# Kernel tuning notes

Hardware: AMD Instinct MI355X
Metric: run time of the kernel (lower is better)

## Reference

```python
import jax, jax.numpy as jnp
import numpy as np

N = 50000
E = 800000
H = 8          # attention heads
C = 16         # per-head channels (128 // 8)
D = 128        # in_channels == num_hidden_channels
L = 2          # num_layers
NEG_SLOPE = 0.2
LN_EPS = 1e-12


def setup_inputs() -> dict:
    key = jax.random.key(0)
    ks = jax.random.split(key, 8)
    x = jax.random.normal(ks[0], (N, D), dtype=jnp.float32)
    edge_index = jax.random.randint(ks[1], (2, E), 0, N).astype(jnp.int64)
    W = jax.random.normal(ks[2], (L, D, D), dtype=jnp.float32) * 0.1
    att = jax.random.normal(ks[3], (L, H, C), dtype=jnp.float32) * 0.1
    bias = jnp.zeros((L, D), dtype=jnp.float32)
    out_W = jax.random.normal(ks[4], (D, D), dtype=jnp.float32) * 0.1
    out_b = jnp.zeros((D,), dtype=jnp.float32)
    ln_g = jnp.ones((D,), dtype=jnp.float32)
    ln_b = jnp.zeros((D,), dtype=jnp.float32)
    return {"x": x, "edge_index": edge_index, "W": W, "att": att, "bias": bias,
            "out_W": out_W, "out_b": out_b, "ln_g": ln_g, "ln_b": ln_b,
            "num_trg_nodes": 25000}


def gatv2_conv(x, src, dst, W_l, a_l, b_l):
    # share_weights=True: same linear map for source and target nodes
    h = (x @ W_l).reshape(N, H, C)               # [N,H,C]
    hs = h[src]                                  # [E,H,C] gather source
    hd = h[dst]                                  # [E,H,C] gather target
    e = jax.nn.leaky_relu(hs + hd, NEG_SLOPE)    # GATv2: LeakyReLU before attention vector
    logits = jnp.einsum('ehc,hc->eh', e, a_l)    # [E,H]
    # segment softmax over edges grouped by destination node
    seg_max = jax.ops.segment_max(logits, dst, num_segments=N)   # [N,H]
    ex = jnp.exp(logits - seg_max[dst])
    seg_sum = jax.ops.segment_sum(ex, dst, num_segments=N)       # [N,H]
    alpha = ex / (seg_sum[dst] + 1e-16)                          # [E,H]
    msg = (hs * alpha[..., None]).reshape(E, H * C)              # weighted messages
    out = jax.ops.segment_sum(msg, dst, num_segments=N)          # [N,H*C]
    return out + b_l


def reference(x, edge_index, W, att, bias, out_W, out_b, ln_g, ln_b, num_trg_nodes):
    src = edge_index[0]
    dst = edge_index[1]
    for i in range(L):
        x = gatv2_conv(x, src, dst, W[i], att[i], bias[i])
        if i != L - 1:
            # eval mode: dropout is identity; torch nn.GELU is exact erf gelu
            x = jax.nn.gelu(x, approximate=False)
    # output head: Linear -> LayerNorm(eps=1e-12) -> Dropout(identity in eval)
    y = x[:num_trg_nodes] @ out_W + out_b
    mu = jnp.mean(y, axis=-1, keepdims=True)
    var = jnp.mean(jnp.square(y - mu), axis=-1, keepdims=True)
    y = (y - mu) / jnp.sqrt(var + LN_EPS) * ln_g + ln_b
    return y
```

## Files before the change

### kernel.cpp

```cpp
#include <hip/hip_runtime.h>
#include <math.h>


#define D 128
#define H 8
#define C 16
#define NBIN 256

typedef __attribute__((ext_vector_type(8))) short bf16x8v;
typedef __attribute__((ext_vector_type(4))) float f32x4v;

static __device__ __forceinline__ float bf2f(unsigned int u16) {
    union { unsigned int i; float f; } x; x.i = u16 << 16; return x.f;
}
static __device__ __forceinline__ unsigned short f2bf(float f) {
    union { float f; unsigned int i; } x; x.f = f;
    unsigned int r = x.i + 0x7fffu + ((x.i >> 16) & 1u);
    return (unsigned short)(r >> 16);
}
static __device__ __forceinline__ float gelu_f(float v) {
    return 0.5f * v * (1.0f + erff(v * 0.70710678118654752f));
}
static __device__ __forceinline__ float exp2_hw(float x) {
    float r;
    asm("v_exp_f32 %0, %1" : "=v"(r) : "v"(x));
    return r;
}
#define DPP_ADD(v, ctrl) \
    (v) += __builtin_bit_cast(float, __builtin_amdgcn_update_dpp( \
        0, __builtin_bit_cast(int, (v)), (ctrl), 0xf, 0xf, true))

template<int IN_BF, int OUT_BF, int GELU>
static __device__ __forceinline__ void gemm_body(
    int bid, const void* __restrict__ Xv, const unsigned short* __restrict__ Wt,
    const float* __restrict__ bias, void* __restrict__ Outv, int nrows)
{
    const int t  = threadIdx.x;
    const int l  = t & 63;
    const int wv = t >> 6;
    const int g  = l >> 4;
    const int r  = l & 15;
    const int m0 = bid * 64;
    const int row = m0 + wv * 16 + r;
    const bool rv = row < nrows;
    const uint4* Wt4 = reinterpret_cast<const uint4*>(Wt);

    bf16x8v afrag[4];
#pragma unroll
    for (int kk = 0; kk < 4; ++kk) {
        int kg = kk * 4 + g;
        float v[8];
        if (IN_BF) {
            uint4 q = make_uint4(0, 0, 0, 0);
            if (rv) q = reinterpret_cast<const uint4*>(Xv)[(size_t)row * 16 + kg];
            if (GELU) {
                unsigned int qq[4] = {q.x, q.y, q.z, q.w};
#pragma unroll
                for (int j = 0; j < 4; ++j) {
                    v[2 * j]     = gelu_f(bf2f(qq[j] & 0xffffu));
                    v[2 * j + 1] = gelu_f(bf2f(qq[j] >> 16));
                }
                short pk[8];
#pragma unroll
                for (int j = 0; j < 8; ++j) pk[j] = (short)f2bf(v[j]);
                afrag[kk] = *reinterpret_cast<bf16x8v*>(pk);
            } else {
                afrag[kk] = __builtin_bit_cast(bf16x8v, q);
            }
        } else {
            float4 a = make_float4(0.f, 0.f, 0.f, 0.f), b = a;
            if (rv) {
                a = reinterpret_cast<const float4*>(Xv)[(size_t)row * 32 + kg * 2];
                b = reinterpret_cast<const float4*>(Xv)[(size_t)row * 32 + kg * 2 + 1];
            }
            v[0] = a.x; v[1] = a.y; v[2] = a.z; v[3] = a.w;
            v[4] = b.x; v[5] = b.y; v[6] = b.z; v[7] = b.w;
            if (GELU) {
#pragma unroll
                for (int j = 0; j < 8; ++j) v[j] = gelu_f(v[j]);
            }
            short pk[8];
#pragma unroll
            for (int j = 0; j < 8; ++j) pk[j] = (short)f2bf(v[j]);
            afrag[kk] = *reinterpret_cast<bf16x8v*>(pk);
        }
    }

    f32x4v acc[8];
#pragma unroll
    for (int ct = 0; ct < 8; ++ct) acc[ct] = (f32x4v){0.f, 0.f, 0.f, 0.f};

    bf16x8v bA[8], bB[8];
#pragma unroll
    for (int ct = 0; ct < 8; ++ct)
        bA[ct] = __builtin_bit_cast(bf16x8v, Wt4[(ct * 16 + r) * 16 + g]);

#pragma unroll
    for (int kk = 0; kk < 4; ++kk) {
        if (kk < 3) {
            int kgn = (kk + 1) * 4 + g;
#pragma unroll
            for (int ct = 0; ct < 8; ++ct) {
                bf16x8v v = __builtin_bit_cast(bf16x8v, Wt4[(ct * 16 + r) * 16 + kgn]);
                if (kk & 1) bA[ct] = v; else bB[ct] = v;
            }
        }
#pragma unroll
        for (int ct = 0; ct < 8; ++ct) {
            bf16x8v b = (kk & 1) ? bB[ct] : bA[ct];
            acc[ct] = __builtin_amdgcn_mfma_f32_16x16x32_bf16(afrag[kk], b, acc[ct], 0, 0, 0);
        }
    }

#pragma unroll
    for (int ct = 0; ct < 8; ++ct) {
        int col = ct * 16 + r;
        float bj = bias ? bias[col] : 0.f;
#pragma unroll
        for (int i = 0; i < 4; ++i) {
            int rr = m0 + wv * 16 + g * 4 + i;
            if (rr < nrows) {
                float val = acc[ct][i] + bj;
                if (OUT_BF)
                    reinterpret_cast<unsigned short*>(Outv)[(size_t)rr * 128 + col] = f2bf(val);
                else
                    reinterpret_cast<float*>(Outv)[(size_t)rr * 128 + col] = val;
            }
        }
    }
}

__global__ __launch_bounds__(256) void gemm_head_ln(
    const void* __restrict__ Xv, const unsigned short* __restrict__ Wt,
    const float* __restrict__ outb, const float* __restrict__ lng,
    const float* __restrict__ lnb, float* __restrict__ Out, int nrows)
{
    const int t  = threadIdx.x;
    const int l  = t & 63;
    const int wv = t >> 6;
    const int g  = l >> 4;
    const int r  = l & 15;
    const int m0 = blockIdx.x * 64;
    const int row = m0 + wv * 16 + r;
    const bool rv = row < nrows;
    const uint4* Wt4 = reinterpret_cast<const uint4*>(Wt);

    bf16x8v afrag[4];
#pragma unroll
    for (int kk = 0; kk < 4; ++kk) {
        int kg = kk * 4 + g;
        uint4 q = make_uint4(0, 0, 0, 0);
        if (rv) q = reinterpret_cast<const uint4*>(Xv)[(size_t)row * 16 + kg];
        afrag[kk] = __builtin_bit_cast(bf16x8v, q);
    }

    f32x4v acc[8];
#pragma unroll
    for (int ct = 0; ct < 8; ++ct) acc[ct] = (f32x4v){0.f, 0.f, 0.f, 0.f};

#pragma unroll
    for (int kk = 0; kk < 4; ++kk) {
        int kg = kk * 4 + g;
#pragma unroll
        for (int ct = 0; ct < 8; ++ct) {
            bf16x8v b = __builtin_bit_cast(bf16x8v, Wt4[(ct * 16 + r) * 16 + kg]);
            acc[ct] = __builtin_amdgcn_mfma_f32_16x16x32_bf16(afrag[kk], b, acc[ct], 0, 0, 0);
        }
    }

    float gmm[8], bbb[8];
#pragma unroll
    for (int ct = 0; ct < 8; ++ct) {
        gmm[ct] = lng[ct * 16 + r];
        bbb[ct] = lnb[ct * 16 + r];
    }

#pragma unroll
    for (int i = 0; i < 4; ++i) {
        int rr = m0 + wv * 16 + g * 4 + i;
        if (rr >= nrows) continue;
        float v[8];
        float s = 0.f;
#pragma unroll
        for (int ct = 0; ct < 8; ++ct) {
            v[ct] = acc[ct][i] + outb[ct * 16 + r];
            s += v[ct];
        }
        DPP_ADD(s, 0xB1); DPP_ADD(s, 0x4E); DPP_ADD(s, 0x141); DPP_ADD(s, 0x140);
        float mu = s * (1.f / 128.f);
        float q = 0.f;
#pragma unroll
        for (int ct = 0; ct < 8; ++ct) {
            float dd = v[ct] - mu;
            q += dd * dd;
        }
        DPP_ADD(q, 0xB1); DPP_ADD(q, 0x4E); DPP_ADD(q, 0x141); DPP_ADD(q, 0x140);
        float inv = rsqrtf(q * (1.f / 128.f) + 1e-12f);
#pragma unroll
        for (int ct = 0; ct < 8; ++ct)
            Out[(size_t)rr * 128 + ct * 16 + r] = (v[ct] - mu) * inv * gmm[ct] + bbb[ct];
    }
}

__global__ __launch_bounds__(256) void prep_kernel(
    const float* __restrict__ W, const float* __restrict__ outW,
    unsigned short* __restrict__ wbf,
    const int* __restrict__ dst, int* __restrict__ bh,
    int E, int chunk, int nblk)
{
    __shared__ char smem[128 * 17 * 2];
    int t = threadIdx.x;
    if (blockIdx.x < 24) {
        unsigned short (*tile)[17] = reinterpret_cast<unsigned short (*)[17]>(smem);
        int blk = blockIdx.x;
        int mat = blk >> 3, s = blk & 7;
        const float* src = (mat < 2) ? (W + (size_t)mat * D * D) : outW;
        unsigned short* dstp = wbf + (size_t)mat * D * D;
        int n0 = s * 16;
#pragma unroll
        for (int it = 0; it < 8; ++it) {
            int idx = it * 256 + t;
            int k = idx >> 4, n = idx & 15;
            tile[k][n] = f2bf(src[k * D + n0 + n]);
        }
        __syncthreads();
#pragma unroll
        for (int it = 0; it < 8; ++it) {
            int idx = it * 256 + t;
            int n = idx >> 7, k = idx & 127;
            dstp[(size_t)(n0 + n) * D + k] = tile[k][n];
        }
    } else {
        int* h = reinterpret_cast<int*>(smem);
        int b = blockIdx.x - 24;
        h[t] = 0;
        __syncthreads();
        int lo = b * chunk, hi = min(E, lo + chunk);
        for (int i = lo + t; i < hi; i += 256) atomicAdd(&h[dst[i] >> 8], 1);
        __syncthreads();
        bh[t * nblk + b] = h[t];
    }
}

__global__ __launch_bounds__(256) void bin_scan(
    int* __restrict__ bh, int* __restrict__ tot, int nblk)
{
    __shared__ int sh[256];
    int bin = blockIdx.x, t = threadIdx.x;
    int v = (t < nblk) ? bh[bin * nblk + t] : 0;
    sh[t] = v;
    __syncthreads();
#pragma unroll
    for (int off = 1; off < 256; off <<= 1) {
        int x = (t >= off) ? sh[t - off] : 0;
        __syncthreads();
        sh[t] += x;
        __syncthreads();
    }
    if (t < nblk) bh[bin * nblk + t] = sh[t] - v;
    if (t == 255) tot[bin] = sh[255];
}

__global__ __launch_bounds__(256) void scatter_gemm0(
    const int* __restrict__ dst, const int* __restrict__ src,
    const int* __restrict__ bh, const int* __restrict__ tot,
    int2* __restrict__ bout, int E, int chunk, int nblk,
    const float* __restrict__ x, const unsigned short* __restrict__ wbf,
    void* __restrict__ hbuf, int nrows)
{
    __shared__ int sh[NBIN];
    __shared__ int cur[NBIN];
    int t = threadIdx.x;
    if (blockIdx.x < nblk) {
        int b = blockIdx.x;
        int tv = tot[t];
        sh[t] = tv;
        __syncthreads();
#pragma unroll
        for (int off = 1; off < 256; off <<= 1) {
            int xq = (t >= off) ? sh[t - off] : 0;
            __syncthreads();
            sh[t] += xq;
            __syncthreads();
        }
        cur[t] = (sh[t] - tv) + bh[t * nblk + b];
        __syncthreads();
        int lo = b * chunk, hi = min(E, lo + chunk);
        for (int i = lo + t; i < hi; i += 256) {
            int d = dst[i];
            int p = atomicAdd(&cur[d >> 8], 1);
            bout[p] = make_int2(src[i], d);
        }
    } else {
        gemm_body<0, 1, 0>(blockIdx.x - nblk, x, wbf, nullptr, hbuf, nrows);
    }
}

__global__ __launch_bounds__(256) void gemm_l1(
    const void* __restrict__ Xv, const unsigned short* __restrict__ Wt,
    void* __restrict__ Outv, int nrows)
{
    gemm_body<1, 1, 1>(blockIdx.x, Xv, Wt, nullptr, Outv, nrows);
}

__global__ __launch_bounds__(256) void fill_fused(
    const int2* __restrict__ bout, const int* __restrict__ tot,
    int* __restrict__ rowptr, int* __restrict__ slist, int N, int E)
{
    __shared__ int sh[NBIN];
    __shared__ int cnt[NBIN];
    __shared__ int cur[NBIN];
    int b = blockIdx.x, t = threadIdx.x;

    int tv = tot[t];
    sh[t] = tv;
    __syncthreads();
#pragma unroll
    for (int off = 1; off < 256; off <<= 1) {
        int x = (t >= off) ? sh[t - off] : 0;
        __syncthreads();
        sh[t] += x;
        __syncthreads();
    }
    int hi = sh[b];
    int lo = hi - tot[b];

    cnt[t] = 0;
    __syncthreads();
    for (int i = lo + t; i < hi; i += 256) atomicAdd(&cnt[bout[i].y & 255], 1);
    __syncthreads();

    int cv = cnt[t];
    sh[t] = cv;
    __syncthreads();
#pragma unroll
    for (int off = 1; off < 256; off <<= 1) {
        int x = (t >= off) ? sh[t - off] : 0;
        __syncthreads();
        sh[t] += x;
        __syncthreads();
    }
    int start = lo + sh[t] - cv;
    int d0 = b * 256 + t;
    if (d0 < N) rowptr[d0] = start;
    if (b == (int)gridDim.x - 1 && t == 255) rowptr[N] = E;
    cur[t] = start;
    __syncthreads();

    for (int i = lo + t; i < hi; i += 256) {
        int2 e = bout[i];
        int p = atomicAdd(&cur[e.y & 255], 1);
        slist[p] = e.x;
    }
}

#define PROC(u, k) \
    float h##k##x = bf2f((u) & 0xffffu), h##k##y = bf2f((u) >> 16); \
    float v##k##0 = h##k##x + hdx, v##k##1 = h##k##y + hdy; \
    float p##k = fmaf(aw1.x, v##k##0, fmaf(aw2.x, fabsf(v##k##0), \
                 fmaf(aw1.y, v##k##1, aw2.y * fabsf(v##k##1)))); \
    DPP_ADD(p##k, 0xB1); DPP_ADD(p##k, 0x4E); DPP_ADD(p##k, 0x141); \
    float e##k = exp2_hw(p##k);

#define QUAD_BODY(U0, U1, U2, U3) \
    { PROC(U0, 0) PROC(U1, 1) PROC(U2, 2) PROC(U3, 3) \
      ssum += (e0 + e1) + (e2 + e3); \
      accx = fmaf(e0, h0x, fmaf(e1, h1x, fmaf(e2, h2x, fmaf(e3, h3x, accx)))); \
      accy = fmaf(e0, h0y, fmaf(e1, h1y, fmaf(e2, h2y, fmaf(e3, h3y, accy)))); }

__global__ __launch_bounds__(256) void aggregate(
    const unsigned int* __restrict__ Hm,
    const int* __restrict__ rowptr, const int* __restrict__ slist,
    const float* __restrict__ att, const float* __restrict__ bias,
    unsigned int* __restrict__ Outv, int n)
{
    int wid  = threadIdx.x >> 6;
    int lane = threadIdx.x & 63;
    int d = blockIdx.x * 4 + wid;
    if (d >= n) return;

    int beg = __builtin_amdgcn_readfirstlane(rowptr[d]);
    int end = __builtin_amdgcn_readfirstlane(rowptr[d + 1]);

    unsigned int ud = Hm[((unsigned)d << 6) | lane];
    float hdx = bf2f(ud & 0xffffu), hdy = bf2f(ud >> 16);
    float2 aw = reinterpret_cast<const float2*>(att)[lane];
    float2 aw1, aw2;
    aw1.x = aw.x * 0.86561702453f;
    aw1.y = aw.y * 0.86561702453f;
    aw2.x = aw.x * 0.57707801636f;
    aw2.y = aw.y * 0.57707801636f;

    float ssum = 0.f, accx = 0.f, accy = 0.f;

    int nfull = (end - beg) >> 2;
    int ii = beg;
    unsigned cu0, cu1, cu2, cu3;
    if (nfull) {
        cu0 = Hm[((unsigned)slist[ii]     << 6) | lane];
        cu1 = Hm[((unsigned)slist[ii + 1] << 6) | lane];
        cu2 = Hm[((unsigned)slist[ii + 2] << 6) | lane];
        cu3 = Hm[((unsigned)slist[ii + 3] << 6) | lane];
    }
    for (int q = 1; q < nfull; ++q) {
        int j = ii + 4;
        unsigned nu0 = Hm[((unsigned)slist[j]     << 6) | lane];
        unsigned nu1 = Hm[((unsigned)slist[j + 1] << 6) | lane];
        unsigned nu2 = Hm[((unsigned)slist[j + 2] << 6) | lane];
        unsigned nu3 = Hm[((unsigned)slist[j + 3] << 6) | lane];
        QUAD_BODY(cu0, cu1, cu2, cu3)
        cu0 = nu0; cu1 = nu1; cu2 = nu2; cu3 = nu3;
        ii = j;
    }
    if (nfull) {
        QUAD_BODY(cu0, cu1, cu2, cu3)
        ii += 4;
    }
    for (; ii < end; ++ii) {
        unsigned u0 = Hm[((unsigned)slist[ii] << 6) | lane];
        PROC(u0, 9)
        ssum += e9;
        accx = fmaf(e9, h9x, accx);
        accy = fmaf(e9, h9y, accy);
    }

    float inv = 1.f / (ssum + 1e-16f);
    float2 bv = reinterpret_cast<const float2*>(bias)[lane];
    float ox = accx * inv + bv.x;
    float oy = accy * inv + bv.y;
    Outv[((unsigned)d << 6) | lane] =
        (unsigned int)f2bf(ox) | ((unsigned int)f2bf(oy) << 16);
}

extern "C" void kernel_launch(void* const* d_in, const int* in_sizes, int n_in,
                              void* d_out, int out_size, void* d_ws, size_t ws_size,
                              hipStream_t stream)
{
    const float* x    = (const float*)d_in[0];
    const int*   edge = (const int*)d_in[1];
    const float* W    = (const float*)d_in[2];
    const float* att  = (const float*)d_in[3];
    const float* bias = (const float*)d_in[4];
    const float* outW = (const float*)d_in[5];
    const float* outb = (const float*)d_in[6];
    const float* lng  = (const float*)d_in[7];
    const float* lnb  = (const float*)d_in[8];

    const int N  = in_sizes[0] / D;
    const int E  = in_sizes[1] / 2;
    const int NT = out_size / D;

    const int* srcp = edge;
    const int* dstp = edge + E;

    auto align256 = [](size_t v) { return (v + 255) & ~(size_t)255; };
    auto cdiv = [](int a, int b) { return (a + b - 1) / b; };

    const int CHUNK = cdiv(E, 256);
    const int NBLK  = cdiv(E, CHUNK);
    const int NBKT  = cdiv(N, 256);
    const int NG    = cdiv(N, 64);

    char* wp = (char*)d_ws;
    size_t off = 0;
    void* hbuf   = (void*)(wp + off); off += align256((size_t)N * D * 2);
    void* xbuf   = (void*)(wp + off); off += align256((size_t)N * D * 2);
    unsigned short* wbf = (unsigned short*)(wp + off); off += align256((size_t)3 * D * D * 2);
    int*  rowptr = (int*)(wp + off);  off += align256((size_t)(N + 1) * 4);
    int*  slist  = (int*)(wp + off);  off += align256((size_t)E * 4);
    int2* bout   = (int2*)(wp + off); off += align256((size_t)E * 8);
    int*  bh     = (int*)(wp + off);  off += align256((size_t)NBIN * NBLK * 4);
    int*  tot    = (int*)(wp + off);  off += align256((size_t)NBIN * 4);
    (void)n_in; (void)ws_size;

    prep_kernel<<<24 + NBLK, 256, 0, stream>>>(W, outW, wbf, dstp, bh, E, CHUNK, NBLK);
    bin_scan<<<NBIN, 256, 0, stream>>>(bh, tot, NBLK);
    scatter_gemm0<<<NBLK + NG, 256, 0, stream>>>(dstp, srcp, bh, tot, bout,
                                                 E, CHUNK, NBLK, x, wbf, hbuf, N);
    fill_fused<<<NBKT, 256, 0, stream>>>(bout, tot, rowptr, slist, N, E);
    aggregate<<<cdiv(N, 4), 256, 0, stream>>>((unsigned int*)hbuf, rowptr, slist,
                                              att, bias, (unsigned int*)xbuf, N);
    gemm_l1<<<NG, 256, 0, stream>>>(xbuf, wbf + D * D, hbuf, N);
    aggregate<<<cdiv(N, 4), 256, 0, stream>>>((unsigned int*)hbuf, rowptr, slist,
                                              att + H * C, bias + D, (unsigned int*)xbuf, N);
    gemm_head_ln<<<cdiv(NT, 64), 256, 0, stream>>>(xbuf, wbf + 2 * D * D, outb,
                                                   lng, lnb, (float*)d_out, NT);
}
```

Measured before the change: 154.6 us.

## Pack bucketed edges into 32-bit words, vectorize edge loads, halve GEMM tile rows

The intermediate bucketed edge buffer now stores src<<8 | (dst&255) in a single 32-bit word instead of an int2, halving its write and read traffic in scatter and fill. The histogram and scatter loops read dst/src as int4 vectors, with CHUNK rounded to a multiple of 4 so the vector loads stay aligned. The GEMM tile shrinks from 64 to 32 rows per block, with each wave pair splitting the 128 output columns, so there are twice as many blocks and fewer accumulator registers per wave. Packing assumes src fits in 24 bits, and the vectorized loop makes each thread handle four edges at a time, changing the order of shared-memory atomic accesses.

```diff
diff --git a/kernel.cpp b/kernel.cpp
--- a/kernel.cpp
+++ b/kernel.cpp
@@ -38,10 +38,12 @@
     const int t  = threadIdx.x;
     const int l  = t & 63;
     const int wv = t >> 6;
+    const int rh = wv >> 1;
+    const int chh = wv & 1;
     const int g  = l >> 4;
     const int r  = l & 15;
-    const int m0 = bid * 64;
-    const int row = m0 + wv * 16 + r;
+    const int m0 = bid * 32 + rh * 16;
+    const int row = m0 + r;
     const bool rv = row < nrows;
     const uint4* Wt4 = reinterpret_cast<const uint4*>(Wt);
 
@@ -86,39 +88,40 @@
         }
     }
 
-    f32x4v acc[8];
-#pragma unroll
-    for (int ct = 0; ct < 8; ++ct) acc[ct] = (f32x4v){0.f, 0.f, 0.f, 0.f};
-
-    bf16x8v bA[8], bB[8];
-#pragma unroll
-    for (int ct = 0; ct < 8; ++ct)
-        bA[ct] = __builtin_bit_cast(bf16x8v, Wt4[(ct * 16 + r) * 16 + g]);
+    f32x4v acc[4];
+#pragma unroll
+    for (int ct = 0; ct < 4; ++ct) acc[ct] = (f32x4v){0.f, 0.f, 0.f, 0.f};
+
+    bf16x8v bA[4], bB[4];
+#pragma unroll
+    for (int ct = 0; ct < 4; ++ct)
+        bA[ct] = __builtin_bit_cast(bf16x8v, Wt4[((chh * 4 + ct) * 16 + r) * 16 + g]);
 
 #pragma unroll
     for (int kk = 0; kk < 4; ++kk) {
         if (kk < 3) {
             int kgn = (kk + 1) * 4 + g;
 #pragma unroll
-            for (int ct = 0; ct < 8; ++ct) {
-                bf16x8v v = __builtin_bit_cast(bf16x8v, Wt4[(ct * 16 + r) * 16 + kgn]);
+            for (int ct = 0; ct < 4; ++ct) {
+                bf16x8v v = __builtin_bit_cast(bf16x8v,
+                    Wt4[((chh * 4 + ct) * 16 + r) * 16 + kgn]);
                 if (kk & 1) bA[ct] = v; else bB[ct] = v;
             }
         }
 #pragma unroll
-        for (int ct = 0; ct < 8; ++ct) {
+        for (int ct = 0; ct < 4; ++ct) {
             bf16x8v b = (kk & 1) ? bB[ct] : bA[ct];
             acc[ct] = __builtin_amdgcn_mfma_f32_16x16x32_bf16(afrag[kk], b, acc[ct], 0, 0, 0);
         }
     }
 
 #pragma unroll
-    for (int ct = 0; ct < 8; ++ct) {
-        int col = ct * 16 + r;
+    for (int ct = 0; ct < 4; ++ct) {
+        int col = (chh * 4 + ct) * 16 + r;
         float bj = bias ? bias[col] : 0.f;
 #pragma unroll
         for (int i = 0; i < 4; ++i) {
-            int rr = m0 + wv * 16 + g * 4 + i;
+            int rr = m0 + g * 4 + i;
             if (rr < nrows) {
                 float val = acc[ct][i] + bj;
                 if (OUT_BF)
@@ -236,7 +239,15 @@
         h[t] = 0;
         __syncthreads();
         int lo = b * chunk, hi = min(E, lo + chunk);
-        for (int i = lo + t; i < hi; i += 256) atomicAdd(&h[dst[i] >> 8], 1);
+        int i = lo + t * 4;
+        for (; i + 3 < hi; i += 1024) {
+            int4 q = *reinterpret_cast<const int4*>(dst + i);
+            atomicAdd(&h[q.x >> 8], 1);
+            atomicAdd(&h[q.y >> 8], 1);
+            atomicAdd(&h[q.z >> 8], 1);
+            atomicAdd(&h[q.w >> 8], 1);
+        }
+        for (; i < hi; ++i) atomicAdd(&h[dst[i] >> 8], 1);
         __syncthreads();
         bh[t * nblk + b] = h[t];
     }
@@ -264,7 +275,7 @@
 __global__ __launch_bounds__(256) void scatter_gemm0(
     const int* __restrict__ dst, const int* __restrict__ src,
     const int* __restrict__ bh, const int* __restrict__ tot,
-    int2* __restrict__ bout, int E, int chunk, int nblk,
+    unsigned int* __restrict__ bout, int E, int chunk, int nblk,
     const float* __restrict__ x, const unsigned short* __restrict__ wbf,
     void* __restrict__ hbuf, int nrows)
 {
@@ -286,10 +297,23 @@
         cur[t] = (sh[t] - tv) + bh[t * nblk + b];
         __syncthreads();
         int lo = b * chunk, hi = min(E, lo + chunk);
-        for (int i = lo + t; i < hi; i += 256) {
+        int i = lo + t * 4;
+        for (; i + 3 < hi; i += 1024) {
+            int4 dq = *reinterpret_cast<const int4*>(dst + i);
+            int4 sq = *reinterpret_cast<const int4*>(src + i);
+            int p0 = atomicAdd(&cur[dq.x >> 8], 1);
+            bout[p0] = ((unsigned)sq.x << 8) | (dq.x & 255);
+            int p1 = atomicAdd(&cur[dq.y >> 8], 1);
+            bout[p1] = ((unsigned)sq.y << 8) | (dq.y & 255);
+            int p2 = atomicAdd(&cur[dq.z >> 8], 1);
+            bout[p2] = ((unsigned)sq.z << 8) | (dq.z & 255);
+            int p3 = atomicAdd(&cur[dq.w >> 8], 1);
+            bout[p3] = ((unsigned)sq.w << 8) | (dq.w & 255);
+        }
+        for (; i < hi; ++i) {
             int d = dst[i];
             int p = atomicAdd(&cur[d >> 8], 1);
-            bout[p] = make_int2(src[i], d);
+            bout[p] = ((unsigned)src[i] << 8) | (d & 255);
         }
     } else {
         gemm_body<0, 1, 0>(blockIdx.x - nblk, x, wbf, nullptr, hbuf, nrows);
@@ -304,7 +328,7 @@
 }
 
 __global__ __launch_bounds__(256) void fill_fused(
-    const int2* __restrict__ bout, const int* __restrict__ tot,
+    const unsigned int* __restrict__ bout, const int* __restrict__ tot,
     int* __restrict__ rowptr, int* __restrict__ slist, int N, int E)
 {
     __shared__ int sh[NBIN];
@@ -327,7 +351,7 @@
 
     cnt[t] = 0;
     __syncthreads();
-    for (int i = lo + t; i < hi; i += 256) atomicAdd(&cnt[bout[i].y & 255], 1);
+    for (int i = lo + t; i < hi; i += 256) atomicAdd(&cnt[bout[i] & 255], 1);
     __syncthreads();
 
     int cv = cnt[t];
@@ -348,9 +372,9 @@
     __syncthreads();
 
     for (int i = lo + t; i < hi; i += 256) {
-        int2 e = bout[i];
-        int p = atomicAdd(&cur[e.y & 255], 1);
-        slist[p] = e.x;
+        unsigned e = bout[i];
+        int p = atomicAdd(&cur[e & 255], 1);
+        slist[p] = (int)(e >> 8);
     }
 }
 
@@ -456,10 +480,10 @@
     auto align256 = [](size_t v) { return (v + 255) & ~(size_t)255; };
     auto cdiv = [](int a, int b) { return (a + b - 1) / b; };
 
-    const int CHUNK = cdiv(E, 256);
+    const int CHUNK = (cdiv(E, 256) + 3) & ~3;
     const int NBLK  = cdiv(E, CHUNK);
     const int NBKT  = cdiv(N, 256);
-    const int NG    = cdiv(N, 64);
+    const int NG    = cdiv(N, 32);
 
     char* wp = (char*)d_ws;
     size_t off = 0;
@@ -468,7 +492,7 @@
     unsigned short* wbf = (unsigned short*)(wp + off); off += align256((size_t)3 * D * D * 2);
     int*  rowptr = (int*)(wp + off);  off += align256((size_t)(N + 1) * 4);
     int*  slist  = (int*)(wp + off);  off += align256((size_t)E * 4);
-    int2* bout   = (int2*)(wp + off); off += align256((size_t)E * 8);
+    unsigned int* bout = (unsigned int*)(wp + off); off += align256((size_t)E * 4);
     int*  bh     = (int*)(wp + off);  off += align256((size_t)NBIN * NBLK * 4);
     int*  tot    = (int*)(wp + off);  off += align256((size_t)NBIN * 4);
     (void)n_in; (void)ws_size;
```

Measured after the change: 151.0 us (median of 2 runs). 2.3% less time.
